# Kernel optimization log

Measured on AMD Instinct MI355X. Metric: run time of the kernel, lower is better.

Reference implementation:

```python
import jax, jax.numpy as jnp
import numpy as np
import math

N_EMBD = 1024
N_HEAD = 16
HEAD_DIM = N_EMBD // N_HEAD
SEQ = 2048
BATCH = 2
EPS = 1e-5


def _gelu_tanh(x):
    c = math.sqrt(2.0 / math.pi)
    return 0.5 * x * (1.0 + jnp.tanh(c * (x + 0.044715 * x ** 3)))


def _layernorm(x, w, b):
    mean = jnp.mean(x, axis=-1, keepdims=True)
    var = jnp.mean(jnp.square(x - mean), axis=-1, keepdims=True)  # unbiased=False
    return (x - mean) / jnp.sqrt(var + EPS) * w + b


def setup_inputs() -> dict:
    key = jax.random.key(0)
    ks = jax.random.split(key, 8)
    D = N_EMBD
    s = 0.02
    return {
        "x": jax.random.normal(ks[0], (BATCH, SEQ, D), jnp.float32),
        "ln1_w": jnp.ones((D,), jnp.float32),
        "ln1_b": jnp.zeros((D,), jnp.float32),
        "w_qkv": jax.random.normal(ks[1], (D, 3 * D), jnp.float32) * s,
        "b_qkv": jnp.zeros((3 * D,), jnp.float32),
        "w_attn_proj": jax.random.normal(ks[2], (D, D), jnp.float32) * s,
        "b_attn_proj": jnp.zeros((D,), jnp.float32),
        "ln2_w": jnp.ones((D,), jnp.float32),
        "ln2_b": jnp.zeros((D,), jnp.float32),
        "w_fc": jax.random.normal(ks[3], (D, 4 * D), jnp.float32) * s,
        "b_fc": jnp.zeros((4 * D,), jnp.float32),
        "w_proj": jax.random.normal(ks[4], (4 * D, D), jnp.float32) * s,
        "b_proj": jnp.zeros((D,), jnp.float32),
    }


def reference(x, ln1_w, ln1_b, w_qkv, b_qkv, w_attn_proj, b_attn_proj,
              ln2_w, ln2_b, w_fc, b_fc, w_proj, b_proj):
    bs, T, D = x.shape
    # --- attention branch (pre-LN) ---
    h = _layernorm(x, ln1_w, ln1_b)
    qkv = h @ w_qkv + b_qkv                      # [B,T,3D]
    q, k, v = jnp.split(qkv, 3, axis=-1)
    q = q.reshape(bs, T, N_HEAD, HEAD_DIM).transpose(0, 2, 1, 3)  # [B,H,T,d]
    k = k.reshape(bs, T, N_HEAD, HEAD_DIM).transpose(0, 2, 1, 3)
    v = v.reshape(bs, T, N_HEAD, HEAD_DIM).transpose(0, 2, 1, 3)
    scores = jnp.einsum("bhqd,bhkd->bhqk", q, k) * (1.0 / math.sqrt(HEAD_DIM))
    causal = jnp.tril(jnp.ones((T, T), bool))
    scores = jnp.where(causal[None, None], scores, -jnp.inf)
    att = jax.nn.softmax(scores, axis=-1)
    ctx = jnp.einsum("bhqk,bhkd->bhqd", att, v)
    ctx = ctx.transpose(0, 2, 1, 3).reshape(bs, T, D)
    attn_out = ctx @ w_attn_proj + b_attn_proj
    x = x + attn_out
    # --- MLP branch (pre-LN) ---
    h = _layernorm(x, ln2_w, ln2_b)
    h = _gelu_tanh(h @ w_fc + b_fc)
    h = h @ w_proj + b_proj
    return x + h
```

## Files before the change

kernel.cpp:

```cpp
#include <hip/hip_runtime.h>

typedef unsigned short u16;
typedef __attribute__((ext_vector_type(8))) __bf16 bf16x8;
typedef __attribute__((ext_vector_type(8))) unsigned short ushort8;
typedef __attribute__((ext_vector_type(4))) float f32x4;

#define MFMA16(a, b, c) __builtin_amdgcn_mfma_f32_16x16x32_bf16((a), (b), (c), 0, 0, 0)

__device__ __forceinline__ u16 f2bf(float f) {
  union { float f; unsigned u; } v; v.f = f;
  unsigned r = v.u + 0x7fffu + ((v.u >> 16) & 1u);
  return (u16)(r >> 16);
}

__device__ __forceinline__ void async16(const u16* g, u16* l) {
  __builtin_amdgcn_global_load_lds(
      (const __attribute__((address_space(1))) void*)g,
      (__attribute__((address_space(3))) void*)l, 16, 0, 0);
}

__global__ __launch_bounds__(256)
void transpose_bf16(const float* __restrict__ W, u16* __restrict__ Wt, int K, int N) {
  __shared__ float t[32][33];
  const int n0 = blockIdx.x * 32, k0 = blockIdx.y * 32;
  const int tx = threadIdx.x, ty = threadIdx.y;
  #pragma unroll
  for (int i = 0; i < 32; i += 8)
    t[ty + i][tx] = W[(size_t)(k0 + ty + i) * N + n0 + tx];
  __syncthreads();
  #pragma unroll
  for (int i = 0; i < 32; i += 8)
    Wt[(size_t)(n0 + ty + i) * K + k0 + tx] = f2bf(t[tx][ty + i]);
}

__global__ __launch_bounds__(256)
void transpose_v(const u16* __restrict__ v, u16* __restrict__ vt) {
  __shared__ u16 t[64][72];
  const int bh = blockIdx.y, t0 = blockIdx.x * 64;
  const int tid = threadIdx.x;
  #pragma unroll
  for (int s = 0; s < 2; ++s) {
    const int idx = tid + s * 256;
    const int row = idx >> 3, ch = idx & 7;
    ushort8 d = *(const ushort8*)(v + ((size_t)bh * 2048 + t0 + row) * 64 + ch * 8);
    #pragma unroll
    for (int e = 0; e < 8; ++e) t[ch * 8 + e][row] = d[e];
  }
  __syncthreads();
  #pragma unroll
  for (int s = 0; s < 2; ++s) {
    const int idx = tid + s * 256;
    const int drow = idx >> 3, ch = idx & 7;
    ushort8 o = *(const ushort8*)(&t[drow][ch * 8]);
    *(ushort8*)(vt + ((size_t)bh * 64 + drow) * 2048 + t0 + ch * 8) = o;
  }
}

__global__ __launch_bounds__(256)
void ln_bf16(const float* __restrict__ X, const float* __restrict__ w,
             const float* __restrict__ bia, u16* __restrict__ out) {
  const int row = blockIdx.x, tid = threadIdx.x;
  const float4 v = ((const float4*)(X + (size_t)row * 1024))[tid];
  float s = v.x + v.y + v.z + v.w;
  float s2 = v.x * v.x + v.y * v.y + v.z * v.z + v.w * v.w;
  #pragma unroll
  for (int o = 32; o > 0; o >>= 1) { s += __shfl_down(s, o); s2 += __shfl_down(s2, o); }
  __shared__ float red[8];
  const int wv = tid >> 6, lane = tid & 63;
  if (lane == 0) { red[wv] = s; red[4 + wv] = s2; }
  __syncthreads();
  s = red[0] + red[1] + red[2] + red[3];
  s2 = red[4] + red[5] + red[6] + red[7];
  const float mean = s * (1.f / 1024.f);
  const float var = s2 * (1.f / 1024.f) - mean * mean;
  const float rstd = rsqrtf(var + 1e-5f);
  const float4 wv4 = ((const float4*)w)[tid];
  const float4 bv4 = ((const float4*)bia)[tid];
  ushort4 o;
  o.x = f2bf((v.x - mean) * rstd * wv4.x + bv4.x);
  o.y = f2bf((v.y - mean) * rstd * wv4.y + bv4.y);
  o.z = f2bf((v.z - mean) * rstd * wv4.z + bv4.z);
  o.w = f2bf((v.w - mean) * rstd * wv4.w + bv4.w);
  ((ushort4*)(out + (size_t)row * 1024))[tid] = o;
}

template <int MODE>
__global__ __launch_bounds__(256)
void gemm_bt(const u16* __restrict__ A, const u16* __restrict__ Bt,
             const float* __restrict__ bias, const float* __restrict__ resid,
             float* __restrict__ outF, u16* __restrict__ outB,
             u16* __restrict__ qo, u16* __restrict__ ko, u16* __restrict__ vo,
             int M, int N, int K) {
  __shared__ u16 As[128 * 32];
  __shared__ u16 Bs[128 * 32];
  const int tid = threadIdx.x;
  const int lane = tid & 63, wv = tid >> 6;
  const int l16 = lane & 15, quad = lane >> 4;
  const int wr = wv >> 1, wc = wv & 1;
  const int m0 = blockIdx.y * 128, n0 = blockIdx.x * 128;
  const int srow = lane >> 2;
  const int scol = (lane & 3) << 3;

  f32x4 acc[4][4];
  const f32x4 fz = {0.f, 0.f, 0.f, 0.f};
  #pragma unroll
  for (int i = 0; i < 4; ++i)
    #pragma unroll
    for (int j = 0; j < 4; ++j) acc[i][j] = fz;

  for (int k0 = 0; k0 < K; k0 += 32) {
    __syncthreads();
    #pragma unroll
    for (int s = 0; s < 2; ++s) {
      const int slot = wv * 2 + s;
      async16(A + (size_t)(m0 + slot * 16 + srow) * K + k0 + scol, As + slot * 512);
      async16(Bt + (size_t)(n0 + slot * 16 + srow) * K + k0 + scol, Bs + slot * 512);
    }
    __builtin_amdgcn_s_waitcnt(0xF70);
    __syncthreads();
    bf16x8 af[4], bfr[4];
    #pragma unroll
    for (int i = 0; i < 4; ++i)
      af[i] = *(const bf16x8*)(As + (wr * 64 + i * 16 + l16) * 32 + quad * 8);
    #pragma unroll
    for (int j = 0; j < 4; ++j)
      bfr[j] = *(const bf16x8*)(Bs + (wc * 64 + j * 16 + l16) * 32 + quad * 8);
    #pragma unroll
    for (int i = 0; i < 4; ++i)
      #pragma unroll
      for (int j = 0; j < 4; ++j)
        acc[i][j] = MFMA16(af[i], bfr[j], acc[i][j]);
  }

  #pragma unroll
  for (int i = 0; i < 4; ++i) {
    #pragma unroll
    for (int j = 0; j < 4; ++j) {
      const int col = n0 + wc * 64 + j * 16 + l16;
      const float bc = bias[col];
      #pragma unroll
      for (int r = 0; r < 4; ++r) {
        const int row = m0 + wr * 64 + i * 16 + quad * 4 + r;
        float v = acc[i][j][r] + bc;
        if (MODE == 0) {
          const int which = col >> 10, cc = col & 1023, hh = cc >> 6, dd = cc & 63;
          const int bb = row >> 11, t = row & 2047;
          const u16 bv = f2bf(v);
          const size_t o = ((size_t)(bb * 16 + hh) * 2048 + t) * 64 + dd;
          if (which == 0) qo[o];
          if (which == 0)
            qo[o] = bv;
          else if (which == 1)
            ko[o] = bv;
          else
            vo[o] = bv;
        } else if (MODE == 1 || MODE == 3) {
          outF[(size_t)row * N + col] = resid[(size_t)row * N + col] + v;
        } else {
          const float x3 = v * v * v;
          const float u = 0.7978845608028654f * (v + 0.044715f * x3);
          const float e = __expf(2.f * u);
          const float th = 1.f - 2.f / (e + 1.f);
          outB[(size_t)row * N + col] = f2bf(0.5f * v * (1.f + th));
        }
      }
    }
  }
}

__global__ __launch_bounds__(256)
void attn(const u16* __restrict__ Q, const u16* __restrict__ Kg,
          const u16* __restrict__ Vt, u16* __restrict__ ctx) {
  __shared__ u16 Ks[128 * 64];
  __shared__ u16 Vs[64 * 128];
  __shared__ u16 Ps[64 * 128];
  const int px = blockIdx.x;
  const int pair = px >> 1, half = px & 1;
  const int qt0 = pair, qt1 = 15 - pair;
  const int bh = blockIdx.y;
  const int b = bh >> 4, h = bh & 15;
  const int tid = threadIdx.x;
  const int lane = tid & 63, wv = tid >> 6;
  const int l16 = lane & 15, quad = lane >> 4;
  const int rb = half * 64 + wv * 16;
  const u16* Qb = Q + (size_t)bh * 2048 * 64;
  const u16* Kb = Kg + (size_t)bh * 2048 * 64;
  const u16* Vb = Vt + (size_t)bh * 64 * 2048;

  bf16x8 qf[2][2];
  #pragma unroll
  for (int t = 0; t < 2; ++t)
    #pragma unroll
    for (int c = 0; c < 2; ++c)
      qf[t][c] = *(const bf16x8*)(Qb + (size_t)((t ? qt1 : qt0) * 128 + rb + l16) * 64 +
                                  c * 32 + quad * 8);

  f32x4 octx[2][4];
  const f32x4 fz = {0.f, 0.f, 0.f, 0.f};
  #pragma unroll
  for (int t = 0; t < 2; ++t)
    #pragma unroll
    for (int jd = 0; jd < 4; ++jd) octx[t][jd] = fz;
  float mi[2][4], li[2][4];
  #pragma unroll
  for (int t = 0; t < 2; ++t)
    #pragma unroll
    for (int r = 0; r < 4; ++r) { mi[t][r] = -1e30f; li[t][r] = 0.f; }

  for (int kt = 0; kt <= qt1; ++kt) {
    __syncthreads();
    #pragma unroll
    for (int s = 0; s < 4; ++s) {
      const int cid = tid + s * 256;
      {
        const int key = cid >> 3, ch = cid & 7;
        ushort8 d = *(const ushort8*)(Kb + (size_t)(kt * 128 + key) * 64 + ch * 8);
        *(ushort8*)(Ks + key * 64 + ((ch ^ (key & 7)) * 8)) = d;
      }
      {
        const int dd = cid >> 4, ch = cid & 15;
        ushort8 d = *(const ushort8*)(Vb + (size_t)dd * 2048 + kt * 128 + ch * 8);
        *(ushort8*)(Vs + dd * 128 + ((ch ^ (dd & 15)) * 8)) = d;
      }
    }
    __syncthreads();

    #pragma unroll
    for (int t = 0; t < 2; ++t) {
      const int qt = t ? qt1 : qt0;
      if (kt > qt) continue;

      f32x4 sa[8];
      #pragma unroll
      for (int j = 0; j < 8; ++j) {
        const int key7 = l16 & 7;
        bf16x8 kf0 = *(const bf16x8*)(Ks + (16 * j + l16) * 64 + ((quad ^ key7) * 8));
        bf16x8 kf1 = *(const bf16x8*)(Ks + (16 * j + l16) * 64 + (((4 + quad) ^ key7) * 8));
        f32x4 tt = MFMA16(qf[t][0], kf0, fz);
        sa[j] = MFMA16(qf[t][1], kf1, tt);
      }
      if (kt == qt) {
        #pragma unroll
        for (int j = 0; j < 8; ++j)
          #pragma unroll
          for (int r = 0; r < 4; ++r) {
            const int rg = rb + quad * 4 + r;
            const int cg = j * 16 + l16;
            if (cg > rg) sa[j][r] = -1e30f;
          }
      }
      #pragma unroll
      for (int r = 0; r < 4; ++r) {
        float mx = -1e30f;
        #pragma unroll
        for (int j = 0; j < 8; ++j) mx = fmaxf(mx, sa[j][r]);
        mx = fmaxf(mx, __shfl_xor(mx, 1));
        mx = fmaxf(mx, __shfl_xor(mx, 2));
        mx = fmaxf(mx, __shfl_xor(mx, 4));
        mx = fmaxf(mx, __shfl_xor(mx, 8));
        mx *= 0.125f;
        const float mn = fmaxf(mi[t][r], mx);
        const float al = __expf(mi[t][r] - mn);
        mi[t][r] = mn;
        const int row = wv * 16 + quad * 4 + r;
        const int rl = row & 15;
        float rs = 0.f;
        #pragma unroll
        for (int j = 0; j < 8; ++j) {
          const float p = __expf(sa[j][r] * 0.125f - mn);
          rs += p;
          const int colc = 2 * j + (l16 >> 3);
          Ps[row * 128 + ((colc ^ rl) * 8) + (l16 & 7)] = f2bf(p);
        }
        rs += __shfl_xor(rs, 1);
        rs += __shfl_xor(rs, 2);
        rs += __shfl_xor(rs, 4);
        rs += __shfl_xor(rs, 8);
        li[t][r] = li[t][r] * al + rs;
        #pragma unroll
        for (int jd = 0; jd < 4; ++jd) octx[t][jd][r] *= al;
      }
      #pragma unroll
      for (int c = 0; c < 4; ++c) {
        const int row = wv * 16 + l16;
        bf16x8 pf = *(const bf16x8*)(Ps + row * 128 + (((c * 4 + quad) ^ l16) * 8));
        #pragma unroll
        for (int jd = 0; jd < 4; ++jd) {
          const int dd = jd * 16 + l16;
          bf16x8 vf = *(const bf16x8*)(Vs + dd * 128 + (((c * 4 + quad) ^ (dd & 15)) * 8));
          octx[t][jd] = MFMA16(pf, vf, octx[t][jd]);
        }
      }
    }
  }
  #pragma unroll
  for (int t = 0; t < 2; ++t) {
    const int qt = t ? qt1 : qt0;
    #pragma unroll
    for (int jd = 0; jd < 4; ++jd)
      #pragma unroll
      for (int r = 0; r < 4; ++r) {
        const int rowg = qt * 128 + rb + quad * 4 + r;
        const int col = h * 64 + jd * 16 + l16;
        ctx[((size_t)b * 2048 + rowg) * 1024 + col] = f2bf(octx[t][jd][r] / li[t][r]);
      }
  }
}

extern "C" void kernel_launch(void* const* d_in, const int* in_sizes, int n_in,
                              void* d_out, int out_size, void* d_ws, size_t ws_size,
                              hipStream_t stream) {
  (void)in_sizes; (void)n_in; (void)out_size; (void)ws_size;
  const float* x      = (const float*)d_in[0];
  const float* ln1_w  = (const float*)d_in[1];
  const float* ln1_b  = (const float*)d_in[2];
  const float* w_qkv  = (const float*)d_in[3];
  const float* b_qkv  = (const float*)d_in[4];
  const float* w_attn = (const float*)d_in[5];
  const float* b_attn = (const float*)d_in[6];
  const float* ln2_w  = (const float*)d_in[7];
  const float* ln2_b  = (const float*)d_in[8];
  const float* w_fc   = (const float*)d_in[9];
  const float* b_fc   = (const float*)d_in[10];
  const float* w_proj = (const float*)d_in[11];
  const float* b_proj = (const float*)d_in[12];
  float* out = (float*)d_out;

  char* ws = (char*)d_ws;
  size_t off = 0;
  auto alloc = [&](size_t n) {
    char* p = ws + off;
    off += (n + 255) & ~(size_t)255;
    return p;
  };
  u16* h1     = (u16*)alloc(4096ull * 1024 * 2);
  u16* wqkvT  = (u16*)alloc(3072ull * 1024 * 2);
  u16* wattnT = (u16*)alloc(1024ull * 1024 * 2);
  u16* wfcT   = (u16*)alloc(4096ull * 1024 * 2);
  u16* wprojT = (u16*)alloc(1024ull * 4096 * 2);
  u16* q      = (u16*)alloc(4096ull * 1024 * 2);
  u16* k      = (u16*)alloc(4096ull * 1024 * 2);
  u16* vT     = (u16*)alloc(4096ull * 1024 * 2);
  u16* ctxb   = (u16*)alloc(4096ull * 1024 * 2);
  float* out1 = (float*)alloc(4096ull * 1024 * 4);
  u16* h2     = (u16*)alloc(4096ull * 1024 * 2);
  u16* fco    = (u16*)alloc(4096ull * 4096 * 2);

  u16* vtmp = ctxb;

  const dim3 tb(32, 8);
  transpose_bf16<<<dim3(3072 / 32, 1024 / 32), tb, 0, stream>>>(w_qkv, wqkvT, 1024, 3072);
  transpose_bf16<<<dim3(1024 / 32, 1024 / 32), tb, 0, stream>>>(w_attn, wattnT, 1024, 1024);
  transpose_bf16<<<dim3(4096 / 32, 1024 / 32), tb, 0, stream>>>(w_fc, wfcT, 1024, 4096);
  transpose_bf16<<<dim3(1024 / 32, 4096 / 32), tb, 0, stream>>>(w_proj, wprojT, 4096, 1024);

  ln_bf16<<<4096, 256, 0, stream>>>(x, ln1_w, ln1_b, h1);

  gemm_bt<0><<<dim3(24, 32), 256, 0, stream>>>(h1, wqkvT, b_qkv, nullptr, nullptr, nullptr,
                                               q, k, vtmp, 4096, 3072, 1024);

  transpose_v<<<dim3(32, 32), 256, 0, stream>>>(vtmp, vT);

  attn<<<dim3(16, 32), 256, 0, stream>>>(q, k, vT, ctxb);

  gemm_bt<1><<<dim3(8, 32), 256, 0, stream>>>(ctxb, wattnT, b_attn, x, out1, nullptr,
                                              nullptr, nullptr, nullptr, 4096, 1024, 1024);

  ln_bf16<<<4096, 256, 0, stream>>>(out1, ln2_w, ln2_b, h2);

  gemm_bt<2><<<dim3(32, 32), 256, 0, stream>>>(h2, wfcT, b_fc, nullptr, nullptr, fco,
                                               nullptr, nullptr, nullptr, 4096, 4096, 1024);

  gemm_bt<3><<<dim3(8, 32), 256, 0, stream>>>(fco, wprojT, b_proj, out1, out, nullptr,
                                              nullptr, nullptr, nullptr, 4096, 1024, 4096);
}
```

Measured before the change: 414.2 us.

## Deepen GEMM K-tile to 64 with XOR-swizzled LDS and split-K the final projection

Raises the GEMM K-step from 32 to 64 and stores the LDS tiles with an XOR swizzle on 16-byte chunks, which halves the number of barrier-separated iterations and avoids LDS bank conflicts on the fragment reads. The MLP down-projection (K=4096, only 256 tiles) is split along K into two slices that write fp32 partials into the reused q buffer. A new reduce kernel then adds the partials, bias and residual. This puts more blocks on the GPU for that GEMM at the cost of an extra fp32 round trip through memory and one more launch. The change also drops a stray dead load in the QKV epilogue.

```diff
diff --git a/kernel.cpp b/kernel.cpp
--- a/kernel.cpp
+++ b/kernel.cpp
@@ -90,16 +90,17 @@
              const float* __restrict__ bias, const float* __restrict__ resid,
              float* __restrict__ outF, u16* __restrict__ outB,
              u16* __restrict__ qo, u16* __restrict__ ko, u16* __restrict__ vo,
-             int M, int N, int K) {
-  __shared__ u16 As[128 * 32];
-  __shared__ u16 Bs[128 * 32];
+             int M, int N, int K, int kSlice) {
+  __shared__ u16 As[128 * 64];
+  __shared__ u16 Bs[128 * 64];
   const int tid = threadIdx.x;
   const int lane = tid & 63, wv = tid >> 6;
   const int l16 = lane & 15, quad = lane >> 4;
   const int wr = wv >> 1, wc = wv & 1;
   const int m0 = blockIdx.y * 128, n0 = blockIdx.x * 128;
-  const int srow = lane >> 2;
-  const int scol = (lane & 3) << 3;
+  const int kBegin = blockIdx.z * kSlice, kEnd = kBegin + kSlice;
+  const int srow = lane >> 3;
+  const int sch = (lane & 7) ^ srow;
 
   f32x4 acc[4][4];
   const f32x4 fz = {0.f, 0.f, 0.f, 0.f};
@@ -108,28 +109,35 @@
     #pragma unroll
     for (int j = 0; j < 4; ++j) acc[i][j] = fz;
 
-  for (int k0 = 0; k0 < K; k0 += 32) {
+  for (int k0 = kBegin; k0 < kEnd; k0 += 64) {
     __syncthreads();
     #pragma unroll
-    for (int s = 0; s < 2; ++s) {
-      const int slot = wv * 2 + s;
-      async16(A + (size_t)(m0 + slot * 16 + srow) * K + k0 + scol, As + slot * 512);
-      async16(Bt + (size_t)(n0 + slot * 16 + srow) * K + k0 + scol, Bs + slot * 512);
+    for (int s = 0; s < 4; ++s) {
+      const int R = wv * 32 + s * 8;
+      async16(A + (size_t)(m0 + R + srow) * K + k0 + sch * 8, As + R * 64);
+      async16(Bt + (size_t)(n0 + R + srow) * K + k0 + sch * 8, Bs + R * 64);
     }
     __builtin_amdgcn_s_waitcnt(0xF70);
     __syncthreads();
-    bf16x8 af[4], bfr[4];
-    #pragma unroll
-    for (int i = 0; i < 4; ++i)
-      af[i] = *(const bf16x8*)(As + (wr * 64 + i * 16 + l16) * 32 + quad * 8);
-    #pragma unroll
-    for (int j = 0; j < 4; ++j)
-      bfr[j] = *(const bf16x8*)(Bs + (wc * 64 + j * 16 + l16) * 32 + quad * 8);
-    #pragma unroll
-    for (int i = 0; i < 4; ++i)
-      #pragma unroll
-      for (int j = 0; j < 4; ++j)
-        acc[i][j] = MFMA16(af[i], bfr[j], acc[i][j]);
+    #pragma unroll
+    for (int h = 0; h < 2; ++h) {
+      bf16x8 af[4], bfr[4];
+      #pragma unroll
+      for (int i = 0; i < 4; ++i) {
+        const int row = wr * 64 + i * 16 + l16;
+        af[i] = *(const bf16x8*)(As + row * 64 + (((h * 4 + quad) ^ (l16 & 7)) * 8));
+      }
+      #pragma unroll
+      for (int j = 0; j < 4; ++j) {
+        const int row = wc * 64 + j * 16 + l16;
+        bfr[j] = *(const bf16x8*)(Bs + row * 64 + (((h * 4 + quad) ^ (l16 & 7)) * 8));
+      }
+      #pragma unroll
+      for (int i = 0; i < 4; ++i)
+        #pragma unroll
+        for (int j = 0; j < 4; ++j)
+          acc[i][j] = MFMA16(af[i], bfr[j], acc[i][j]);
+    }
   }
 
   #pragma unroll
@@ -141,31 +149,50 @@
       #pragma unroll
       for (int r = 0; r < 4; ++r) {
         const int row = m0 + wr * 64 + i * 16 + quad * 4 + r;
-        float v = acc[i][j][r] + bc;
+        float v = acc[i][j][r];
+        if (MODE != 4) v += bc;
         if (MODE == 0) {
           const int which = col >> 10, cc = col & 1023, hh = cc >> 6, dd = cc & 63;
           const int bb = row >> 11, t = row & 2047;
           const u16 bv = f2bf(v);
           const size_t o = ((size_t)(bb * 16 + hh) * 2048 + t) * 64 + dd;
-          if (which == 0) qo[o];
           if (which == 0)
             qo[o] = bv;
           else if (which == 1)
             ko[o] = bv;
           else
             vo[o] = bv;
-        } else if (MODE == 1 || MODE == 3) {
+        } else if (MODE == 1) {
           outF[(size_t)row * N + col] = resid[(size_t)row * N + col] + v;
-        } else {
+        } else if (MODE == 2) {
           const float x3 = v * v * v;
           const float u = 0.7978845608028654f * (v + 0.044715f * x3);
           const float e = __expf(2.f * u);
           const float th = 1.f - 2.f / (e + 1.f);
           outB[(size_t)row * N + col] = f2bf(0.5f * v * (1.f + th));
+        } else {
+          outF[(size_t)blockIdx.z * M * N + (size_t)row * N + col] = v;
         }
       }
     }
   }
+}
+
+__global__ __launch_bounds__(256)
+void reduce2(const float* __restrict__ P, const float* __restrict__ resid,
+             const float* __restrict__ bias, float* __restrict__ out, int MN, int N) {
+  const int idx4 = blockIdx.x * 256 + threadIdx.x;
+  const size_t s = (size_t)MN >> 2;
+  const float4 a = ((const float4*)P)[idx4];
+  const float4 b = ((const float4*)P)[idx4 + s];
+  const float4 r = ((const float4*)resid)[idx4];
+  const float4 bb = ((const float4*)bias)[idx4 & (N / 4 - 1)];
+  float4 o;
+  o.x = r.x + a.x + b.x + bb.x;
+  o.y = r.y + a.y + b.y + bb.y;
+  o.z = r.z + a.z + b.z + bb.z;
+  o.w = r.w + a.w + b.w + bb.w;
+  ((float4*)out)[idx4] = o;
 }
 
 __global__ __launch_bounds__(256)
@@ -347,6 +374,7 @@
   u16* fco    = (u16*)alloc(4096ull * 4096 * 2);
 
   u16* vtmp = ctxb;
+  float* projP = (float*)q;
 
   const dim3 tb(32, 8);
   transpose_bf16<<<dim3(3072 / 32, 1024 / 32), tb, 0, stream>>>(w_qkv, wqkvT, 1024, 3072);
@@ -356,21 +384,23 @@
 
   ln_bf16<<<4096, 256, 0, stream>>>(x, ln1_w, ln1_b, h1);
 
-  gemm_bt<0><<<dim3(24, 32), 256, 0, stream>>>(h1, wqkvT, b_qkv, nullptr, nullptr, nullptr,
-                                               q, k, vtmp, 4096, 3072, 1024);
+  gemm_bt<0><<<dim3(24, 32, 1), 256, 0, stream>>>(h1, wqkvT, b_qkv, nullptr, nullptr,
+                                                  nullptr, q, k, vtmp, 4096, 3072, 1024, 1024);
 
   transpose_v<<<dim3(32, 32), 256, 0, stream>>>(vtmp, vT);
 
   attn<<<dim3(16, 32), 256, 0, stream>>>(q, k, vT, ctxb);
 
-  gemm_bt<1><<<dim3(8, 32), 256, 0, stream>>>(ctxb, wattnT, b_attn, x, out1, nullptr,
-                                              nullptr, nullptr, nullptr, 4096, 1024, 1024);
+  gemm_bt<1><<<dim3(8, 32, 1), 256, 0, stream>>>(ctxb, wattnT, b_attn, x, out1, nullptr,
+                                                 nullptr, nullptr, nullptr, 4096, 1024, 1024, 1024);
 
   ln_bf16<<<4096, 256, 0, stream>>>(out1, ln2_w, ln2_b, h2);
 
-  gemm_bt<2><<<dim3(32, 32), 256, 0, stream>>>(h2, wfcT, b_fc, nullptr, nullptr, fco,
-                                               nullptr, nullptr, nullptr, 4096, 4096, 1024);
-
-  gemm_bt<3><<<dim3(8, 32), 256, 0, stream>>>(fco, wprojT, b_proj, out1, out, nullptr,
-                                              nullptr, nullptr, nullptr, 4096, 1024, 4096);
-}
+  gemm_bt<2><<<dim3(32, 32, 1), 256, 0, stream>>>(h2, wfcT, b_fc, nullptr, nullptr, fco,
+                                                  nullptr, nullptr, nullptr, 4096, 4096, 1024, 1024);
+
+  gemm_bt<4><<<dim3(8, 32, 2), 256, 0, stream>>>(fco, wprojT, b_proj, nullptr, projP, nullptr,
+                                                 nullptr, nullptr, nullptr, 4096, 1024, 4096, 2048);
+
+  reduce2<<<4096, 256, 0, stream>>>(projP, out1, b_proj, out, 4096 * 1024, 1024);
+}
```

New measurement: 383.8 us. -7.3%, faster.
